# Kernel tuning notes

Hardware: AMD Instinct MI355X
Metric: run time of the kernel (lower is better)

Reference implementation:

```python
import jax, jax.numpy as jnp
import numpy as np

N = 100000
E = 800000
D_IN = 128
D_OUT = 128
EPS = 1e-5


def setup_inputs() -> dict:
    key = jax.random.key(0)
    k = jax.random.split(key, 7)
    x = jax.random.normal(k[0], (N, D_IN), dtype=jnp.float32)
    edge_index = jax.random.randint(k[1], (2, E), 0, N, dtype=jnp.int64)
    # kaiming_uniform(a=sqrt(5)) on [out,in] -> bound = 1/sqrt(in_dim)
    bound = 1.0 / np.sqrt(D_IN)
    W_self = jax.random.uniform(k[2], (D_OUT, D_IN), minval=-bound, maxval=bound, dtype=jnp.float32)
    W_neigh = jax.random.uniform(k[3], (D_OUT, D_IN), minval=-bound, maxval=bound, dtype=jnp.float32)
    bias = jnp.zeros((D_OUT,), dtype=jnp.float32)
    gamma = jnp.ones((D_OUT,), dtype=jnp.float32)
    beta = jnp.zeros((D_OUT,), dtype=jnp.float32)
    return {"x": x, "edge_index": edge_index, "W_self": W_self,
            "W_neigh": W_neigh, "bias": bias, "gamma": gamma, "beta": beta}


def reference(x, edge_index, W_self, W_neigh, bias, gamma, beta):
    src, dst = edge_index[0], edge_index[1]
    # mean neighbor aggregation: segment-sum of gathered features / clamped degree
    agg = jax.ops.segment_sum(x[src], dst, num_segments=N)          # [N, D_IN]
    deg = jax.ops.segment_sum(jnp.ones_like(dst, dtype=x.dtype), dst, num_segments=N)
    neigh_mean = agg / jnp.maximum(deg, 1.0)[:, None]
    # dual linear + bias + ReLU
    out = jnp.einsum('nd,od->no', x, W_self) + jnp.einsum('nd,od->no', neigh_mean, W_neigh) + bias
    h = jax.nn.relu(out)
    # LayerNorm over last dim
    mu = jnp.mean(h, axis=-1, keepdims=True)
    var = jnp.var(h, axis=-1, keepdims=True)
    return (h - mu) * jax.lax.rsqrt(var + EPS) * gamma + beta
```

## Files before the change

### kernel.cpp

```cpp
#include <hip/hip_runtime.h>
#include <hip/hip_bf16.h>

#define N_NODES 100000
#define E_EDGES 800000
#define CAP 32
#define LN_EPS 1e-5f
#define WPAD 264
#define NBK 256
#define NSLICE 391
#define BKCAP 4096
#define EPB 3125
#define MAGIC391 10984572ULL
#define CONV_PER_BLOCK 12500

typedef __attribute__((ext_vector_type(4))) float f32x4;
typedef __attribute__((ext_vector_type(8))) short short8;

__device__ __forceinline__ unsigned short f2bf(float f) {
    __hip_bfloat16 h = __float2bfloat16(f);
    return *reinterpret_cast<unsigned short*>(&h);
}
__device__ __forceinline__ float bflo(unsigned int u) { return __uint_as_float(u << 16); }
__device__ __forceinline__ float bfhi(unsigned int u) { return __uint_as_float(u & 0xffff0000u); }

__global__ __launch_bounds__(256) void fill_part1(
    const float* __restrict__ x, const int* __restrict__ ei,
    unsigned short* __restrict__ xb, unsigned long long* __restrict__ gstore,
    int* __restrict__ gcursor)
{
    const int t = threadIdx.x, b = blockIdx.x;
    if (b >= NBK) {
        const float4* x4 = reinterpret_cast<const float4*>(x);
        ushort4* xb4 = reinterpret_cast<ushort4*>(xb);
        const int j0 = (b - NBK) * CONV_PER_BLOCK;
        for (int j = t; j < CONV_PER_BLOCK; j += 256) {
            float4 v = x4[j0 + j];
            ushort4 o;
            o.x = f2bf(v.x); o.y = f2bf(v.y); o.z = f2bf(v.z); o.w = f2bf(v.w);
            xb4[j0 + j] = o;
        }
        return;
    }
    __shared__ unsigned long long eds[EPB];
    __shared__ int hist[NBK], base_[NBK], run[NBK];
    hist[t] = 0; run[t] = 0;
    __syncthreads();
    const int e0 = b * EPB;
    for (int i = t; i < EPB; i += 256) {
        unsigned src = (unsigned)ei[e0 + i];
        unsigned dst = (unsigned)ei[E_EDGES + e0 + i];
        unsigned bk = (unsigned)((dst * MAGIC391) >> 32);
        unsigned low = dst - bk * NSLICE;
        eds[i] = ((unsigned long long)((bk << 16) | low) << 32) | src;
        atomicAdd(&hist[bk], 1);
    }
    __syncthreads();
    base_[t] = atomicAdd(&gcursor[t], hist[t]);
    __syncthreads();
    for (int i = t; i < EPB; i += 256) {
        unsigned long long u = eds[i];
        unsigned bk = (unsigned)(u >> 48);
        int p = base_[bk] + atomicAdd(&run[bk], 1);
        if (p < BKCAP)
            gstore[bk * BKCAP + p] = u & 0x0000ffffffffffffULL;
    }
}

__global__ __launch_bounds__(256) void fill_part2(
    const unsigned long long* __restrict__ gstore, const int* __restrict__ gcursor,
    int* __restrict__ cnt, int* __restrict__ slots)
{
    __shared__ int cnt_l[NSLICE];
    __shared__ int slots_l[NSLICE * CAP];
    const int t = threadIdx.x, b = blockIdx.x;
    const int base = b * NSLICE;
    for (int i = t; i < NSLICE; i += 256) cnt_l[i] = 0;
    __syncthreads();
    int n = gcursor[b];
    if (n > BKCAP) n = BKCAP;
    const unsigned long long* bs = gstore + b * BKCAP;
    for (int i = t; i < n; i += 256) {
        unsigned long long u = bs[i];
        unsigned low = (unsigned)(u >> 32);
        int p = atomicAdd(&cnt_l[low], 1);
        if (p < CAP) slots_l[low * CAP + p] = (int)(unsigned)u;
    }
    __syncthreads();
    for (int i = t; i < NSLICE; i += 256) cnt[base + i] = cnt_l[i];
    for (int i = t; i < NSLICE * CAP; i += 256) slots[base * CAP + i] = slots_l[i];
}

__global__ __launch_bounds__(256) void gather_kernel(
    const unsigned short* __restrict__ xb, const int* __restrict__ cnt,
    const int* __restrict__ slots, unsigned short* __restrict__ nb)
{
    int node = (blockIdx.x * blockDim.x + threadIdx.x) >> 6;
    int lane = threadIdx.x & 63;
    if (node >= N_NODES) return;
    int c = cnt[node];
    int cc = c > CAP ? CAP : c;
    int myslot = (lane < cc) ? slots[node * CAP + lane] : 0;
    const int subi = lane >> 4, chunk = lane & 15;
    float acc[8];
#pragma unroll
    for (int k = 0; k < 8; ++k) acc[k] = 0.f;
    const uint4* x4 = reinterpret_cast<const uint4*>(xb);
    for (int i = 0; i < cc; i += 4) {
        int idx = i + subi;
        int s = __shfl(myslot, idx);
        uint4 v = x4[s * 16 + chunk];
        if (idx < cc) {
            acc[0] += bflo(v.x); acc[1] += bfhi(v.x);
            acc[2] += bflo(v.y); acc[3] += bfhi(v.y);
            acc[4] += bflo(v.z); acc[5] += bfhi(v.z);
            acc[6] += bflo(v.w); acc[7] += bfhi(v.w);
        }
    }
#pragma unroll
    for (int k = 0; k < 8; ++k) {
        acc[k] += __shfl_xor(acc[k], 16);
        acc[k] += __shfl_xor(acc[k], 32);
    }
    if (subi == 0) {
        float inv = 1.0f / (float)(c > 1 ? c : 1);
        uint4 o;
        o.x = ((unsigned)f2bf(acc[1] * inv) << 16) | f2bf(acc[0] * inv);
        o.y = ((unsigned)f2bf(acc[3] * inv) << 16) | f2bf(acc[2] * inv);
        o.z = ((unsigned)f2bf(acc[5] * inv) << 16) | f2bf(acc[4] * inv);
        o.w = ((unsigned)f2bf(acc[7] * inv) << 16) | f2bf(acc[6] * inv);
        reinterpret_cast<uint4*>(nb)[node * 16 + chunk] = o;
    }
}

__global__ __launch_bounds__(256, 2) void fused_mfma(
    const unsigned short* __restrict__ xb, const unsigned short* __restrict__ nb,
    const float* __restrict__ Wself, const float* __restrict__ Wneigh,
    const float* __restrict__ bias, const float* __restrict__ gamma,
    const float* __restrict__ beta, float* __restrict__ out)
{
    __shared__ unsigned short WT[128][WPAD];
    const int t = threadIdx.x;
    const float4* Ws4 = reinterpret_cast<const float4*>(Wself);
    const float4* Wn4 = reinterpret_cast<const float4*>(Wneigh);
    for (int idx = t; idx < 4096; idx += 256) {
        int n = idx >> 5, k4 = (idx & 31) << 2;
        float4 a = Ws4[idx];
        float4 b = Wn4[idx];
        ushort4 ua, ub;
        ua.x = f2bf(a.x); ua.y = f2bf(a.y); ua.z = f2bf(a.z); ua.w = f2bf(a.w);
        ub.x = f2bf(b.x); ub.y = f2bf(b.y); ub.z = f2bf(b.z); ub.w = f2bf(b.w);
        *reinterpret_cast<ushort4*>(&WT[n][k4]) = ua;
        *reinterpret_cast<ushort4*>(&WT[n][128 + k4]) = ub;
    }
    __syncthreads();

    const int lane = t & 63, wave = t >> 6;
    const int l16 = lane & 15, quad = lane >> 4;
    float bia[8], gam[8], bet[8];
#pragma unroll
    for (int n = 0; n < 8; ++n) {
        int col = n * 16 + l16;
        bia[n] = bias[col]; gam[n] = gamma[col]; bet[n] = beta[col];
    }

    const int ntiles = (N_NODES + 255) / 256;
    for (int tile = blockIdx.x; tile < ntiles; tile += gridDim.x) {
        const int rowbase = tile * 256 + wave * 64;
        f32x4 acc[4][8];
#pragma unroll
        for (int m = 0; m < 4; ++m)
#pragma unroll
            for (int n = 0; n < 8; ++n) acc[m][n] = (f32x4)0.f;
        int rows[4];
#pragma unroll
        for (int m = 0; m < 4; ++m) {
            int r = rowbase + m * 16 + l16;
            rows[m] = r < N_NODES ? r : N_NODES - 1;
        }
#pragma unroll
        for (int kstep = 0; kstep < 8; ++kstep) {
            const unsigned short* Asrc = (kstep < 4) ? xb : nb;
            const int koff = (kstep & 3) * 32 + quad * 8;
            short8 a[4];
#pragma unroll
            for (int m = 0; m < 4; ++m)
                a[m] = *reinterpret_cast<const short8*>(Asrc + rows[m] * 128 + koff);
#pragma unroll
            for (int n = 0; n < 8; ++n) {
                short8 b = *reinterpret_cast<const short8*>(&WT[n * 16 + l16][kstep * 32 + quad * 8]);
#pragma unroll
                for (int m = 0; m < 4; ++m)
                    acc[m][n] = __builtin_amdgcn_mfma_f32_16x16x32_bf16(a[m], b, acc[m][n], 0, 0, 0);
            }
        }
#pragma unroll
        for (int m = 0; m < 4; ++m) {
#pragma unroll
            for (int r = 0; r < 4; ++r) {
                float h[8], s = 0.f, q = 0.f;
#pragma unroll
                for (int n = 0; n < 8; ++n) {
                    float v = acc[m][n][r] + bia[n];
                    v = fmaxf(v, 0.f);
                    h[n] = v; s += v; q += v * v;
                }
#pragma unroll
                for (int msk = 1; msk <= 8; msk <<= 1) {
                    s += __shfl_xor(s, msk);
                    q += __shfl_xor(q, msk);
                }
                const float mu = s * (1.f / 128.f);
                const float var = q * (1.f / 128.f) - mu * mu;
                const float rs = rsqrtf(var + LN_EPS);
                const int R = rowbase + m * 16 + quad * 4 + r;
                if (R < N_NODES) {
#pragma unroll
                    for (int n = 0; n < 8; ++n)
                        out[R * 128 + n * 16 + l16] = (h[n] - mu) * rs * gam[n] + bet[n];
                }
            }
        }
    }
}

extern "C" void kernel_launch(void* const* d_in, const int* in_sizes, int n_in,
                              void* d_out, int out_size, void* d_ws, size_t ws_size,
                              hipStream_t stream) {
    const float* x      = (const float*)d_in[0];
    const int*   ei     = (const int*)d_in[1];
    const float* Wself  = (const float*)d_in[2];
    const float* Wneigh = (const float*)d_in[3];
    const float* bias   = (const float*)d_in[4];
    const float* gamma  = (const float*)d_in[5];
    const float* beta   = (const float*)d_in[6];
    float* out = (float*)d_out;

    char* ws = (char*)d_ws;
    unsigned short* xb = (unsigned short*)ws;
    int* cnt   = (int*)(ws + 25600000);
    int* slots = (int*)(ws + 26000384);
    unsigned long long* gstore = (unsigned long long*)(ws + 38812672);
    unsigned short* nb = (unsigned short*)(ws + 38812672);
    int* gcursor = (int*)(ws + 64412672);

    hipMemsetAsync(gcursor, 0, NBK * sizeof(int), stream);
    fill_part1<<<512, 256, 0, stream>>>(x, ei, xb, gstore, gcursor);
    fill_part2<<<NBK, 256, 0, stream>>>(gstore, gcursor, cnt, slots);
    gather_kernel<<<(N_NODES + 3) / 4, 256, 0, stream>>>(xb, cnt, slots, nb);
    const int ntiles = (N_NODES + 255) / 256;
    fused_mfma<<<ntiles, 256, 0, stream>>>(xb, nb, Wself, Wneigh, bias, gamma, beta, out);
}
```

Baseline: 210.4 us.

## Replace atomic bucket scatter with per-block sorted runs and fused per-slice aggregation

Each edge partition block now locally counting-sorts its edges by 64-node destination slices and writes the sorted run together with per-slice offsets. A new aggregation kernel, one block per slice, collects the matching run segments from all 256 partitions, sorts them by node in shared memory, and gathers the bf16 features directly. This removes the memset, the global cursor atomics, the intermediate slots/count arrays and one kernel launch. It also drops the per-node cap of 32 neighbours, replacing it with a per-slice cap of 768 edges. In exchange, each agg2 thread serially reads one partition's run, and slices with fewer than 64 nodes' worth of work leave many waves idle.

```diff
diff --git a/kernel.cpp b/kernel.cpp
--- a/kernel.cpp
+++ b/kernel.cpp
@@ -3,14 +3,16 @@
 
 #define N_NODES 100000
 #define E_EDGES 800000
-#define CAP 32
 #define LN_EPS 1e-5f
 #define WPAD 264
-#define NBK 256
-#define NSLICE 391
-#define BKCAP 4096
+
+#define P_BLOCKS 256
 #define EPB 3125
-#define MAGIC391 10984572ULL
+#define SLICE 64
+#define NBK 1563
+#define NBK_PAD 1792
+#define OFFS_STRIDE 1564
+#define QCAP 768
 #define CONV_PER_BLOCK 12500
 
 typedef __attribute__((ext_vector_type(4))) float f32x4;
@@ -25,14 +27,14 @@
 
 __global__ __launch_bounds__(256) void fill_part1(
     const float* __restrict__ x, const int* __restrict__ ei,
-    unsigned short* __restrict__ xb, unsigned long long* __restrict__ gstore,
-    int* __restrict__ gcursor)
+    unsigned short* __restrict__ xb, unsigned int* __restrict__ gstore,
+    unsigned short* __restrict__ offs)
 {
     const int t = threadIdx.x, b = blockIdx.x;
-    if (b >= NBK) {
+    if (b >= P_BLOCKS) {
         const float4* x4 = reinterpret_cast<const float4*>(x);
         ushort4* xb4 = reinterpret_cast<ushort4*>(xb);
-        const int j0 = (b - NBK) * CONV_PER_BLOCK;
+        const int j0 = (b - P_BLOCKS) * CONV_PER_BLOCK;
         for (int j = t; j < CONV_PER_BLOCK; j += 256) {
             float4 v = x4[j0 + j];
             ushort4 o;
@@ -42,93 +44,119 @@
         return;
     }
     __shared__ unsigned long long eds[EPB];
-    __shared__ int hist[NBK], base_[NBK], run[NBK];
-    hist[t] = 0; run[t] = 0;
+    __shared__ unsigned int sorted_l[EPB];
+    __shared__ int hist[NBK_PAD];
+    __shared__ int starts[NBK_PAD + 1];
+    __shared__ int partial[256];
+    for (int i = t; i < NBK_PAD; i += 256) hist[i] = 0;
     __syncthreads();
     const int e0 = b * EPB;
     for (int i = t; i < EPB; i += 256) {
         unsigned src = (unsigned)ei[e0 + i];
         unsigned dst = (unsigned)ei[E_EDGES + e0 + i];
-        unsigned bk = (unsigned)((dst * MAGIC391) >> 32);
-        unsigned low = dst - bk * NSLICE;
-        eds[i] = ((unsigned long long)((bk << 16) | low) << 32) | src;
+        unsigned bk = dst >> 6;
+        eds[i] = ((unsigned long long)bk << 32) | (src << 6) | (dst & 63u);
         atomicAdd(&hist[bk], 1);
     }
     __syncthreads();
-    base_[t] = atomicAdd(&gcursor[t], hist[t]);
+    int h[7], s = 0;
+#pragma unroll
+    for (int k = 0; k < 7; ++k) { h[k] = hist[t * 7 + k]; s += h[k]; }
+    partial[t] = s;
+    __syncthreads();
+    for (int off = 1; off < 256; off <<= 1) {
+        int v = (t >= off) ? partial[t - off] : 0;
+        __syncthreads();
+        partial[t] += v;
+        __syncthreads();
+    }
+    int run = partial[t] - s;
+#pragma unroll
+    for (int k = 0; k < 7; ++k) { starts[t * 7 + k] = run; run += h[k]; }
+    if (t == 255) starts[NBK_PAD] = run;
+    __syncthreads();
+    for (int i = t; i < NBK_PAD; i += 256) hist[i] = 0;
     __syncthreads();
     for (int i = t; i < EPB; i += 256) {
         unsigned long long u = eds[i];
-        unsigned bk = (unsigned)(u >> 48);
-        int p = base_[bk] + atomicAdd(&run[bk], 1);
-        if (p < BKCAP)
-            gstore[bk * BKCAP + p] = u & 0x0000ffffffffffffULL;
-    }
-}
-
-__global__ __launch_bounds__(256) void fill_part2(
-    const unsigned long long* __restrict__ gstore, const int* __restrict__ gcursor,
-    int* __restrict__ cnt, int* __restrict__ slots)
+        unsigned bk = (unsigned)(u >> 32);
+        int p = starts[bk] + atomicAdd(&hist[bk], 1);
+        sorted_l[p] = (unsigned int)u;
+    }
+    __syncthreads();
+    for (int i = t; i < EPB; i += 256)
+        gstore[b * EPB + i] = sorted_l[i];
+    for (int i = t; i < OFFS_STRIDE; i += 256)
+        offs[b * OFFS_STRIDE + i] = (unsigned short)starts[i];
+}
+
+__global__ __launch_bounds__(256) void agg2(
+    const unsigned int* __restrict__ gstore, const unsigned short* __restrict__ offs,
+    const unsigned short* __restrict__ xb, unsigned short* __restrict__ nb)
 {
-    __shared__ int cnt_l[NSLICE];
-    __shared__ int slots_l[NSLICE * CAP];
+    __shared__ unsigned int sortedq[QCAP];
+    __shared__ int cnt_l[SLICE];
+    __shared__ int run_l[SLICE];
+    __shared__ int qs_l[SLICE + 1];
     const int t = threadIdx.x, b = blockIdx.x;
-    const int base = b * NSLICE;
-    for (int i = t; i < NSLICE; i += 256) cnt_l[i] = 0;
-    __syncthreads();
-    int n = gcursor[b];
-    if (n > BKCAP) n = BKCAP;
-    const unsigned long long* bs = gstore + b * BKCAP;
-    for (int i = t; i < n; i += 256) {
-        unsigned long long u = bs[i];
-        unsigned low = (unsigned)(u >> 32);
-        int p = atomicAdd(&cnt_l[low], 1);
-        if (p < CAP) slots_l[low * CAP + p] = (int)(unsigned)u;
-    }
-    __syncthreads();
-    for (int i = t; i < NSLICE; i += 256) cnt[base + i] = cnt_l[i];
-    for (int i = t; i < NSLICE * CAP; i += 256) slots[base * CAP + i] = slots_l[i];
-}
-
-__global__ __launch_bounds__(256) void gather_kernel(
-    const unsigned short* __restrict__ xb, const int* __restrict__ cnt,
-    const int* __restrict__ slots, unsigned short* __restrict__ nb)
-{
-    int node = (blockIdx.x * blockDim.x + threadIdx.x) >> 6;
-    int lane = threadIdx.x & 63;
-    if (node >= N_NODES) return;
-    int c = cnt[node];
-    int cc = c > CAP ? CAP : c;
-    int myslot = (lane < cc) ? slots[node * CAP + lane] : 0;
+    if (t < SLICE) { cnt_l[t] = 0; run_l[t] = 0; }
+    __syncthreads();
+    const int s0 = offs[t * OFFS_STRIDE + b];
+    const int s1 = offs[t * OFFS_STRIDE + b + 1];
+    const unsigned int* myrun = gstore + t * EPB;
+    for (int j = s0; j < s1; ++j)
+        atomicAdd(&cnt_l[myrun[j] & 63u], 1);
+    __syncthreads();
+    if (t < SLICE) {
+        int inc = cnt_l[t];
+        for (int off = 1; off < 64; off <<= 1) {
+            int u = __shfl_up(inc, off);
+            if (t >= off) inc += u;
+        }
+        qs_l[t + 1] = inc;
+        if (t == 0) qs_l[0] = 0;
+    }
+    __syncthreads();
+    for (int j = s0; j < s1; ++j) {
+        unsigned rec = myrun[j];
+        int p = qs_l[rec & 63u] + atomicAdd(&run_l[rec & 63u], 1);
+        if (p < QCAP) sortedq[p] = rec;
+    }
+    __syncthreads();
+    const int wave = t >> 6, lane = t & 63;
     const int subi = lane >> 4, chunk = lane & 15;
-    float acc[8];
-#pragma unroll
-    for (int k = 0; k < 8; ++k) acc[k] = 0.f;
     const uint4* x4 = reinterpret_cast<const uint4*>(xb);
-    for (int i = 0; i < cc; i += 4) {
-        int idx = i + subi;
-        int s = __shfl(myslot, idx);
-        uint4 v = x4[s * 16 + chunk];
-        if (idx < cc) {
-            acc[0] += bflo(v.x); acc[1] += bfhi(v.x);
-            acc[2] += bflo(v.y); acc[3] += bfhi(v.y);
-            acc[4] += bflo(v.z); acc[5] += bfhi(v.z);
-            acc[6] += bflo(v.w); acc[7] += bfhi(v.w);
-        }
-    }
-#pragma unroll
-    for (int k = 0; k < 8; ++k) {
-        acc[k] += __shfl_xor(acc[k], 16);
-        acc[k] += __shfl_xor(acc[k], 32);
-    }
-    if (subi == 0) {
-        float inv = 1.0f / (float)(c > 1 ? c : 1);
-        uint4 o;
-        o.x = ((unsigned)f2bf(acc[1] * inv) << 16) | f2bf(acc[0] * inv);
-        o.y = ((unsigned)f2bf(acc[3] * inv) << 16) | f2bf(acc[2] * inv);
-        o.z = ((unsigned)f2bf(acc[5] * inv) << 16) | f2bf(acc[4] * inv);
-        o.w = ((unsigned)f2bf(acc[7] * inv) << 16) | f2bf(acc[6] * inv);
-        reinterpret_cast<uint4*>(nb)[node * 16 + chunk] = o;
+    for (int ln = wave * 16; ln < wave * 16 + 16; ++ln) {
+        const int qb = qs_l[ln], cc = qs_l[ln + 1] - qb;
+        float acc[8];
+#pragma unroll
+        for (int k = 0; k < 8; ++k) acc[k] = 0.f;
+        for (int i = 0; i < cc; i += 4) {
+            int idx = i + subi;
+            if (idx < cc) {
+                unsigned rec = sortedq[qb + idx];
+                uint4 v = x4[(rec >> 6) * 16 + chunk];
+                acc[0] += bflo(v.x); acc[1] += bfhi(v.x);
+                acc[2] += bflo(v.y); acc[3] += bfhi(v.y);
+                acc[4] += bflo(v.z); acc[5] += bfhi(v.z);
+                acc[6] += bflo(v.w); acc[7] += bfhi(v.w);
+            }
+        }
+#pragma unroll
+        for (int k = 0; k < 8; ++k) {
+            acc[k] += __shfl_xor(acc[k], 16);
+            acc[k] += __shfl_xor(acc[k], 32);
+        }
+        const int node = b * SLICE + ln;
+        if (subi == 0 && node < N_NODES) {
+            float inv = 1.0f / (float)(cc > 1 ? cc : 1);
+            uint4 o;
+            o.x = ((unsigned)f2bf(acc[1] * inv) << 16) | f2bf(acc[0] * inv);
+            o.y = ((unsigned)f2bf(acc[3] * inv) << 16) | f2bf(acc[2] * inv);
+            o.z = ((unsigned)f2bf(acc[5] * inv) << 16) | f2bf(acc[4] * inv);
+            o.w = ((unsigned)f2bf(acc[7] * inv) << 16) | f2bf(acc[6] * inv);
+            reinterpret_cast<uint4*>(nb)[node * 16 + chunk] = o;
+        }
     }
 }
 
@@ -237,16 +265,12 @@
 
     char* ws = (char*)d_ws;
     unsigned short* xb = (unsigned short*)ws;
-    int* cnt   = (int*)(ws + 25600000);
-    int* slots = (int*)(ws + 26000384);
-    unsigned long long* gstore = (unsigned long long*)(ws + 38812672);
-    unsigned short* nb = (unsigned short*)(ws + 38812672);
-    int* gcursor = (int*)(ws + 64412672);
-
-    hipMemsetAsync(gcursor, 0, NBK * sizeof(int), stream);
-    fill_part1<<<512, 256, 0, stream>>>(x, ei, xb, gstore, gcursor);
-    fill_part2<<<NBK, 256, 0, stream>>>(gstore, gcursor, cnt, slots);
-    gather_kernel<<<(N_NODES + 3) / 4, 256, 0, stream>>>(xb, cnt, slots, nb);
+    unsigned short* nb = (unsigned short*)(ws + 25600000);
+    unsigned int* gstore = (unsigned int*)(ws + 51200000);
+    unsigned short* offs = (unsigned short*)(ws + 54400000);
+
+    fill_part1<<<512, 256, 0, stream>>>(x, ei, xb, gstore, offs);
+    agg2<<<NBK, 256, 0, stream>>>(gstore, offs, xb, nb);
     const int ntiles = (N_NODES + 255) / 256;
     fused_mfma<<<ntiles, 256, 0, stream>>>(xb, nb, Wself, Wneigh, bias, gamma, beta, out);
 }
```

After: 204.8 us. 2.7% less time.
